# Kernel optimization log

Measured on AMD Instinct MI355X. Metric: run time of the kernel, lower is better.

## Reference

```python
import jax, jax.numpy as jnp
import numpy as np

V, D, G = 128000, 2048, 32  # vocab, embedding dim, int4 group size
B, S = 8, 4096
QMIN, QMAX = -8, 7  # int4 range (bit_width=4)


def setup_inputs() -> dict:
    key = jax.random.key(0)
    k1, k2, k3, k4 = jax.random.split(key, 4)
    # int4 values stored in int8-like container: range [-8, 7]
    weight = jax.random.randint(k1, (V, D), 0, 16, dtype=jnp.int32) - 8
    scale = jax.random.uniform(k2, (V, D // G), dtype=jnp.float32) * 0.02 + 1e-3
    zero_point = jax.random.randint(k3, (V, D // G), 0, 16, dtype=jnp.int32) - 8
    x = jax.random.randint(k4, (B, S), 0, V, dtype=jnp.int64)
    return {"weight": weight, "scale": scale, "zero_point": zero_point, "x": x}


def reference(weight, scale, zero_point, x):
    # Group-wise dequant: (w - zero_point) * scale, per group of G channels,
    # matching _quantized_decomposed_dequantize_per_channel_group.
    n_groups = scale.shape[1]
    g = weight.shape[1] // n_groups  # group_size
    w = weight.reshape(weight.shape[0], n_groups, g).astype(scale.dtype)
    zp = zero_point.reshape(zero_point.shape[0], n_groups, 1).astype(scale.dtype)
    w_dq = ((w - zp) * scale[:, :, None]).reshape(weight.shape)  # [V, D]
    # F.embedding with padding_idx=None, max_norm=None is a plain gather
    return w_dq[x]  # [B, S, D]
```

## Files before the change

kernel.cpp:

```cpp
#include <hip/hip_runtime.h>


#define DIM 2048
#define NGROUPS 64

__global__ __launch_bounds__(256) void int4_embed_dequant_kernel(
    const int* __restrict__ weight,
    const float* __restrict__ scale,
    const int* __restrict__ zp,
    const int* __restrict__ x,
    float* __restrict__ out,
    int n_tokens)
{
    const int token = blockIdx.x;
    if (token >= n_tokens) return;

    const int row = x[token];
    const int t = threadIdx.x;
    const int d0 = t << 3;
    const int g = d0 >> 5;

    const size_t srow = (size_t)row * NGROUPS + g;
    const float s = scale[srow];
    const float z = (float)zp[srow];

    const int4* __restrict__ wrow =
        (const int4*)weight + (size_t)row * (DIM / 4) + (t << 1);
    float4* __restrict__ orow =
        (float4*)out + (size_t)token * (DIM / 4) + (t << 1);

    const int4 w0 = wrow[0];
    const int4 w1 = wrow[1];

    float4 o0, o1;
    o0.x = ((float)w0.x - z) * s;
    o0.y = ((float)w0.y - z) * s;
    o0.z = ((float)w0.z - z) * s;
    o0.w = ((float)w0.w - z) * s;
    o1.x = ((float)w1.x - z) * s;
    o1.y = ((float)w1.y - z) * s;
    o1.z = ((float)w1.z - z) * s;
    o1.w = ((float)w1.w - z) * s;

    orow[0] = o0;
    orow[1] = o1;
}

extern "C" void kernel_launch(void* const* d_in, const int* in_sizes, int n_in,
                              void* d_out, int out_size, void* d_ws, size_t ws_size,
                              hipStream_t stream) {
    const int* weight  = (const int*)d_in[0];
    const float* scale = (const float*)d_in[1];
    const int* zp      = (const int*)d_in[2];
    const int* x       = (const int*)d_in[3];

    float* out = (float*)d_out;

    const int n_tokens = in_sizes[3];

    dim3 grid(n_tokens);
    dim3 block(256);
    int4_embed_dequant_kernel<<<grid, block, 0, stream>>>(
        weight, scale, zp, x, out, n_tokens);
}
```

Measured before the change: 106.3 us.

## Use persistent grid-stride blocks with index prefetch and nontemporal output stores

```diff
diff --git a/kernel.cpp b/kernel.cpp
--- a/kernel.cpp
+++ b/kernel.cpp
@@ -3,6 +3,9 @@
 
 #define DIM 2048
 #define NGROUPS 64
+
+typedef float  f32x4 __attribute__((ext_vector_type(4)));
+typedef int    i32x4 __attribute__((ext_vector_type(4)));
 
 __global__ __launch_bounds__(256) void int4_embed_dequant_kernel(
     const int* __restrict__ weight,
@@ -12,38 +15,48 @@
     float* __restrict__ out,
     int n_tokens)
 {
-    const int token = blockIdx.x;
+    const int t = threadIdx.x;
+    const int g = t >> 2;
+    const int stride = gridDim.x;
+
+    int token = blockIdx.x;
     if (token >= n_tokens) return;
 
-    const int row = x[token];
-    const int t = threadIdx.x;
-    const int d0 = t << 3;
-    const int g = d0 >> 5;
+    int row = x[token];
 
-    const size_t srow = (size_t)row * NGROUPS + g;
-    const float s = scale[srow];
-    const float z = (float)zp[srow];
+    while (token < n_tokens) {
+        const int next_token = token + stride;
+        int next_row = 0;
+        if (next_token < n_tokens) next_row = x[next_token];
 
-    const int4* __restrict__ wrow =
-        (const int4*)weight + (size_t)row * (DIM / 4) + (t << 1);
-    float4* __restrict__ orow =
-        (float4*)out + (size_t)token * (DIM / 4) + (t << 1);
+        const size_t srow = (size_t)row * NGROUPS + g;
+        const float s = scale[srow];
+        const float z = (float)zp[srow];
 
-    const int4 w0 = wrow[0];
-    const int4 w1 = wrow[1];
+        const i32x4* __restrict__ wrow =
+            (const i32x4*)weight + (size_t)row * (DIM / 4) + (t << 1);
+        f32x4* orow =
+            (f32x4*)out + (size_t)token * (DIM / 4) + (t << 1);
 
-    float4 o0, o1;
-    o0.x = ((float)w0.x - z) * s;
-    o0.y = ((float)w0.y - z) * s;
-    o0.z = ((float)w0.z - z) * s;
-    o0.w = ((float)w0.w - z) * s;
-    o1.x = ((float)w1.x - z) * s;
-    o1.y = ((float)w1.y - z) * s;
-    o1.z = ((float)w1.z - z) * s;
-    o1.w = ((float)w1.w - z) * s;
+        const i32x4 w0 = wrow[0];
+        const i32x4 w1 = wrow[1];
 
-    orow[0] = o0;
-    orow[1] = o1;
+        f32x4 o0, o1;
+        o0.x = ((float)w0.x - z) * s;
+        o0.y = ((float)w0.y - z) * s;
+        o0.z = ((float)w0.z - z) * s;
+        o0.w = ((float)w0.w - z) * s;
+        o1.x = ((float)w1.x - z) * s;
+        o1.y = ((float)w1.y - z) * s;
+        o1.z = ((float)w1.z - z) * s;
+        o1.w = ((float)w1.w - z) * s;
+
+        __builtin_nontemporal_store(o0, orow);
+        __builtin_nontemporal_store(o1, orow + 1);
+
+        token = next_token;
+        row = next_row;
+    }
 }
 
 extern "C" void kernel_launch(void* const* d_in, const int* in_sizes, int n_in,
@@ -58,8 +71,9 @@
 
     const int n_tokens = in_sizes[3];
 
-    dim3 grid(n_tokens);
-    dim3 block(256);
-    int4_embed_dequant_kernel<<<grid, block, 0, stream>>>(
+    int grid = 2048;
+    if (grid > n_tokens) grid = n_tokens;
+
+    int4_embed_dequant_kernel<<<dim3(grid), dim3(256), 0, stream>>>(
         weight, scale, zp, x, out, n_tokens);
 }
```

Measured after the change: 98.68 us. -7.2%, faster.
